# Performance work log

Hardware: AMD Instinct MI355X
Metric: run time of the kernel (lower is better)

The kernel has to match this reference:

```python
import jax, jax.numpy as jnp
import numpy as np

SEGMENT_LENGTHS = [1024, 2048, 4096]
DILATION_RATES = [1, 2, 4]


def setup_inputs() -> dict:
    key = jax.random.key(0)
    k1, k2, k3 = jax.random.split(key, 3)
    n = sum(SEGMENT_LENGTHS)  # 7168
    shape = (1, n, 8, 64)  # (b, n, h, d)
    q = jax.random.normal(k1, shape, dtype=jnp.float32)
    k = jax.random.normal(k2, shape, dtype=jnp.float32)
    v = jax.random.normal(k3, shape, dtype=jnp.float32)
    return {"q": q, "k": k, "v": v}


def _attend(q_seg, k_kv, v_kv):
    # q_seg: [b, q_len, h, d]; k_kv/v_kv: [b, k_len, h, d]
    d = q_seg.shape[-1]
    scale = 1.0 / jnp.sqrt(jnp.asarray(d, q_seg.dtype))
    scores = jnp.einsum("bqhd,bkhd->bhqk", q_seg, k_kv) * scale
    w = jax.nn.softmax(scores, axis=-1)
    return jnp.einsum("bhqk,bkhd->bqhd", w, v_kv)


def reference(q, k, v):
    # Single-device dilated attention (ring_size == 1, is_causal=False).
    n = q.shape[1]
    output = jnp.zeros_like(q)
    seg_start = 0
    for seg_len, dilation in zip(SEGMENT_LENGTHS, DILATION_RATES):
        if seg_start >= n:
            break
        seg_end = min(seg_start + seg_len, n)
        q_seg = q[:, seg_start:seg_end]
        if dilation > 1:
            k_d = k[:, ::dilation]
            v_d = v[:, ::dilation]
        else:
            k_d, v_d = k, v
        out_seg = _attend(q_seg, k_d, v_d)
        output = output.at[:, seg_start:seg_end].set(out_seg)
        seg_start = seg_end
    return output
```

## Files before the change

### kernel.cpp

```cpp
#include <hip/hip_runtime.h>

#define VB0 3670016L
#define VB1 7340032L
#define VB2 9175040L
#define WS_SHORTS 10092544L
#define PO_OFF 5046272L
#define PL_OFF (PO_OFF + 512L * 128 * 64)

typedef short bvec8 __attribute__((ext_vector_type(8)));
typedef float fvec16 __attribute__((ext_vector_type(16)));

static __device__ __forceinline__ short f2bf(float f) {
  unsigned u = __float_as_uint(f);
  u = u + 0x7fffu + ((u >> 16) & 1u);
  return (short)(u >> 16);
}
static __device__ __forceinline__ unsigned pk2(float a, float b) {
  unsigned ua = (__float_as_uint(a) + 0x8000u) >> 16;
  unsigned ub = (__float_as_uint(b) + 0x8000u) & 0xffff0000u;
  return ua | ub;
}
static __device__ __forceinline__ void async16(const short* g, short* l) {
  __builtin_amdgcn_global_load_lds((const __attribute__((address_space(1))) unsigned*)(void*)g,
                                   (__attribute__((address_space(3))) unsigned*)(void*)l, 16, 0, 0);
}

__global__ __launch_bounds__(256) void pack_all(const float* __restrict__ k,
                                                const float* __restrict__ v,
                                                short* __restrict__ W) {
  __shared__ float tl[64][65];
  int b = blockIdx.x, t = threadIdx.x;
  if (b < 896) {
    int h = b / 112, tile = b % 112, i0 = tile * 64;
    int r = t >> 2, c = t & 3;
    const float* src = k + ((long)(i0 + r) * 8 + h) * 64 + c * 16;
    short* dst = W + ((long)h * 7168 + i0 + r) * 64 + c * 16;
    short tmp[16] __attribute__((aligned(16)));
#pragma unroll
    for (int q4 = 0; q4 < 4; q4++) {
      float4 x = *(const float4*)(src + q4 * 4);
      tmp[q4 * 4 + 0] = f2bf(x.x); tmp[q4 * 4 + 1] = f2bf(x.y);
      tmp[q4 * 4 + 2] = f2bf(x.z); tmp[q4 * 4 + 3] = f2bf(x.w);
    }
    *(bvec8*)dst = *(const bvec8*)tmp;
    *(bvec8*)(dst + 8) = *(const bvec8*)(tmp + 8);
  } else {
    int b2 = b - 896;
    int h, tile, dil, L; long base;
    if (b2 < 896)       { L = 7168; dil = 1; h = b2 / 112; tile = b2 % 112; base = VB0; }
    else if (b2 < 1344) { int bb = b2 - 896;  L = 3584; dil = 2; h = bb / 56; tile = bb % 56; base = VB1; }
    else                { int bb = b2 - 1344; L = 1792; dil = 4; h = bb / 28; tile = bb % 28; base = VB2; }
    int i0 = tile * 64;
    int row = t >> 2, c = t & 3;
    const float* src = v + ((long)(i0 + row) * dil * 8 + h) * 64;
#pragma unroll
    for (int cc = 0; cc < 4; cc++) {
      int d0 = c * 16 + cc * 4;
      float4 x = *(const float4*)(src + d0);
      tl[row][d0 + 0] = x.x; tl[row][d0 + 1] = x.y;
      tl[row][d0 + 2] = x.z; tl[row][d0 + 3] = x.w;
    }
    __syncthreads();
    int d = t >> 2, part = t & 3;
    short tmp[16] __attribute__((aligned(16)));
#pragma unroll
    for (int u = 0; u < 16; u++) tmp[u] = f2bf(tl[part * 16 + u][d]);
    short* dst = W + base + ((long)h * 64 + d) * L + i0 + part * 16;
    *(bvec8*)dst = *(const bvec8*)tmp;
    *(bvec8*)(dst + 8) = *(const bvec8*)(tmp + 8);
  }
}

__global__ __launch_bounds__(256, 3) void attn_kern(const float* __restrict__ q,
                                                    const short* __restrict__ W,
                                                    float* __restrict__ out,
                                                    float* __restrict__ PO,
                                                    float* __restrict__ PL) {
  int b = blockIdx.x;
  int h, q0, dil, kt0, L; long vbo;
  if (b < 256)      { int sp = b & 3; h = (b >> 2) & 7; int qt = b >> 5;
                      q0 = qt * 128;        dil = 1; L = 7168; vbo = VB0; kt0 = sp * 28; }
  else if (b < 512) { int i = b - 256; int sp = i & 1; h = (i >> 1) & 7; int qt = i >> 4;
                      q0 = 1024 + qt * 128; dil = 2; L = 3584; vbo = VB1; kt0 = sp * 28; }
  else              { int i = b - 512; h = i & 7; int qt = i >> 3;
                      q0 = 3072 + qt * 128; dil = 4; L = 1792; vbo = VB2; kt0 = 0; }
  const short* kb = W + (long)h * 7168 * 64;
  const short* vt = W + vbo + (long)h * 64 * L;
  const int dil64 = dil * 64;

  __shared__ __attribute__((aligned(16))) short sK[2][4096];
  __shared__ __attribute__((aligned(16))) short sV[2][4096];
  short* sKf = &sK[0][0];
  short* sVf = &sV[0][0];

  int t = threadIdx.x, lane = t & 63, w = t >> 6;
  int ln = lane & 31, hb = lane >> 5;

  bvec8 qb[4];
  {
    const float* qp = q + ((long)(q0 + w * 32 + ln) * 8 + h) * 64 + 8 * hb;
    const float qs = 0.125f * 1.44269504088896f;
#pragma unroll
    for (int ks = 0; ks < 4; ks++)
#pragma unroll
      for (int j = 0; j < 8; j++)
        qb[ks][j] = f2bf(qs * qp[ks * 16 + j]);
  }

  int srow = lane >> 3, sch = (lane & 7) ^ srow;
  auto stage = [&](int keybase, int buf) {
#pragma unroll
    for (int r2 = 0; r2 < 2; r2++) {
      int row = (w * 2 + r2) * 8 + srow;
      const short* gpk = kb + (long)(keybase + row) * dil64 + sch * 8;
      async16(gpk, sKf + (long)buf * 4096 + (w * 2 + r2) * 512);
      const short* gpv = vt + (long)row * L + keybase + sch * 8;
      async16(gpv, sVf + (long)buf * 4096 + (w * 2 + r2) * 512);
    }
  };

  stage(kt0 * 64, 0);

  int koff[8];
#pragma unroll
  for (int ks = 0; ks < 4; ks++)
#pragma unroll
    for (int mb = 0; mb < 2; mb++)
      koff[ks * 2 + mb] = (mb * 32 + ln) * 64 + (((2 * ks + hb) ^ (ln & 7)) * 8);

  fvec16 Oa[2];
#pragma unroll
  for (int i = 0; i < 16; i++) { Oa[0][i] = 0.f; Oa[1][i] = 0.f; }
  float lp = 0.f;

  for (int it = 0; it < 28; it++) {
    int buf = it & 1;
    int key0 = (kt0 + it) * 64;
    __syncthreads();

    if (it < 27) stage(key0 + 64, buf ^ 1);

    fvec16 Sa[2];
#pragma unroll
    for (int i = 0; i < 16; i++) { Sa[0][i] = 0.f; Sa[1][i] = 0.f; }
    const short* sb = sKf + (long)buf * 4096;
#pragma unroll
    for (int ks = 0; ks < 4; ks++)
#pragma unroll
      for (int mb = 0; mb < 2; mb++) {
        bvec8 kf = *(const bvec8*)(sb + koff[ks * 2 + mb]);
        Sa[mb] = __builtin_amdgcn_mfma_f32_32x32x16_bf16(kf, qb[ks], Sa[mb], 0, 0, 0);
      }

    const short* vbuf = sVf + (long)buf * 4096;
    bvec8 vf[8];
#pragma unroll
    for (int ks = 0; ks < 4; ks++)
#pragma unroll
      for (int mb = 0; mb < 2; mb++)
        vf[mb * 4 + ks] = *(const bvec8*)(vbuf + koff[ks * 2 + mb]);

#pragma unroll
    for (int ks2 = 0; ks2 < 4; ks2++) {
      int mb = ks2 >> 1, r0i = (ks2 & 1) * 8;
      float p[8];
#pragma unroll
      for (int u = 0; u < 8; u++) {
        p[u] = __builtin_amdgcn_exp2f(Sa[mb][r0i + u]);
        lp += p[u];
      }
      unsigned da0 = pk2(p[0], p[1]), da1 = pk2(p[2], p[3]);
      unsigned db0 = pk2(p[4], p[5]), db1 = pk2(p[6], p[7]);
      unsigned s0 = hb ? da0 : db0, s1 = hb ? da1 : db1;
      unsigned x0 = __shfl_xor(s0, 32), x1 = __shfl_xor(s1, 32);
      union { unsigned u[4]; bvec8 v; } fu;
      fu.u[0] = hb ? x0 : da0;  fu.u[1] = hb ? x1 : da1;
      fu.u[2] = hb ? db0 : x0;  fu.u[3] = hb ? db1 : x1;
#pragma unroll
      for (int mb2 = 0; mb2 < 2; mb2++)
        Oa[mb2] = __builtin_amdgcn_mfma_f32_32x32x16_bf16(vf[mb2 * 4 + ks2], fu.v, Oa[mb2], 0, 0, 0);
    }
  }

  float lf = lp + __shfl_xor(lp, 32);
  int wl = w * 32 + ln;
  if (b < 512) {
    float* po = PO + ((long)b * 128 + wl) * 64;
#pragma unroll
    for (int mb2 = 0; mb2 < 2; mb2++)
#pragma unroll
      for (int r2 = 0; r2 < 4; r2++) {
        float4 x = { Oa[mb2][r2 * 4 + 0], Oa[mb2][r2 * 4 + 1],
                     Oa[mb2][r2 * 4 + 2], Oa[mb2][r2 * 4 + 3] };
        *(float4*)(po + mb2 * 32 + r2 * 8 + hb * 4) = x;
      }
    if (hb == 0) PL[(long)b * 128 + wl] = lf;
  } else {
    float inv = 1.f / lf;
    float* op = out + ((long)(q0 + wl) * 8 + h) * 64;
#pragma unroll
    for (int mb2 = 0; mb2 < 2; mb2++)
#pragma unroll
      for (int r2 = 0; r2 < 4; r2++) {
        float4 x = { Oa[mb2][r2 * 4 + 0] * inv, Oa[mb2][r2 * 4 + 1] * inv,
                     Oa[mb2][r2 * 4 + 2] * inv, Oa[mb2][r2 * 4 + 3] * inv };
        *(float4*)(op + mb2 * 32 + r2 * 8 + hb * 4) = x;
      }
  }
}

__global__ __launch_bounds__(256) void combine_kern(const float* __restrict__ PO,
                                                    const float* __restrict__ PL,
                                                    float* __restrict__ out) {
  int g = blockIdx.x, t = threadIdx.x;
  int base_b, nsp, q0, h;
  if (g < 64) { int qt = g >> 3; h = g & 7; base_b = qt * 32 + h * 4; nsp = 4; q0 = qt * 128; }
  else { int gi = g - 64; int qt = gi >> 3; h = gi & 7; base_b = 256 + qt * 16 + h * 2; nsp = 2; q0 = 1024 + qt * 128; }
  int r = t >> 1, ch = (t & 1) * 32;
  float lt = 0.f;
  for (int sp = 0; sp < nsp; sp++) lt += PL[(long)(base_b + sp) * 128 + r];
  float inv = 1.f / lt;
  float4 acc[8];
#pragma unroll
  for (int j = 0; j < 8; j++) { acc[j].x = 0.f; acc[j].y = 0.f; acc[j].z = 0.f; acc[j].w = 0.f; }
  for (int sp = 0; sp < nsp; sp++) {
    const float4* pb = (const float4*)(PO + ((long)(base_b + sp) * 128 + r) * 64 + ch);
#pragma unroll
    for (int j = 0; j < 8; j++) {
      float4 x = pb[j];
      acc[j].x += x.x; acc[j].y += x.y; acc[j].z += x.z; acc[j].w += x.w;
    }
  }
  float4* op = (float4*)(out + ((long)(q0 + r) * 8 + h) * 64 + ch);
#pragma unroll
  for (int j = 0; j < 8; j++) {
    float4 x = { acc[j].x * inv, acc[j].y * inv, acc[j].z * inv, acc[j].w * inv };
    op[j] = x;
  }
}

extern "C" void kernel_launch(void* const* d_in, const int* in_sizes, int n_in,
                              void* d_out, int out_size, void* d_ws, size_t ws_size,
                              hipStream_t stream) {
  const float* q = (const float*)d_in[0];
  const float* k = (const float*)d_in[1];
  const float* v = (const float*)d_in[2];
  float* out = (float*)d_out;
  short* W = (short*)d_ws;
  float* PO = (float*)d_ws + PO_OFF;
  float* PL = (float*)d_ws + PL_OFF;

  pack_all<<<2464, 256, 0, stream>>>(k, v, W);
  attn_kern<<<768, 256, 0, stream>>>(q, W, out, PO, PL);
  combine_kern<<<192, 256, 0, stream>>>(PO, PL, out);
}
```

Measured before the change: 160.9 us.

## Halve attention block to two waves, single-buffer V, split row-sum accumulators

The attention kernel now runs 128-thread blocks, each covering 64 query rows, so the grid doubles to 1536 blocks and the partial-output buffers and combine kernel are resized to match. V is single-buffered in shared memory: its fragments are loaded into registers before an added barrier, and only then is the next tile prefetched, which lowers LDS per block so more blocks fit per CU. The softmax row sum is split into four independent accumulators to shorten the dependency chain. The cost is an extra barrier per iteration, a less hidden V prefetch, and Q staging and partial writes repeated across twice as many blocks.

```diff
diff --git a/kernel.cpp b/kernel.cpp
--- a/kernel.cpp
+++ b/kernel.cpp
@@ -3,9 +3,8 @@
 #define VB0 3670016L
 #define VB1 7340032L
 #define VB2 9175040L
-#define WS_SHORTS 10092544L
 #define PO_OFF 5046272L
-#define PL_OFF (PO_OFF + 512L * 128 * 64)
+#define PL_OFF (PO_OFF + 1024L * 64 * 64)
 
 typedef short bvec8 __attribute__((ext_vector_type(8)));
 typedef float fvec16 __attribute__((ext_vector_type(16)));
@@ -71,27 +70,26 @@
   }
 }
 
-__global__ __launch_bounds__(256, 3) void attn_kern(const float* __restrict__ q,
+__global__ __launch_bounds__(128, 3) void attn_kern(const float* __restrict__ q,
                                                     const short* __restrict__ W,
                                                     float* __restrict__ out,
                                                     float* __restrict__ PO,
                                                     float* __restrict__ PL) {
   int b = blockIdx.x;
   int h, q0, dil, kt0, L; long vbo;
-  if (b < 256)      { int sp = b & 3; h = (b >> 2) & 7; int qt = b >> 5;
-                      q0 = qt * 128;        dil = 1; L = 7168; vbo = VB0; kt0 = sp * 28; }
-  else if (b < 512) { int i = b - 256; int sp = i & 1; h = (i >> 1) & 7; int qt = i >> 4;
-                      q0 = 1024 + qt * 128; dil = 2; L = 3584; vbo = VB1; kt0 = sp * 28; }
-  else              { int i = b - 512; h = i & 7; int qt = i >> 3;
-                      q0 = 3072 + qt * 128; dil = 4; L = 1792; vbo = VB2; kt0 = 0; }
+  if (b < 512)       { int sp = b & 3; h = (b >> 2) & 7; int qt = b >> 5;
+                       q0 = qt * 64;         dil = 1; L = 7168; vbo = VB0; kt0 = sp * 28; }
+  else if (b < 1024) { int i = b - 512; int sp = i & 1; h = (i >> 1) & 7; int qt = i >> 4;
+                       q0 = 1024 + qt * 64;  dil = 2; L = 3584; vbo = VB1; kt0 = sp * 28; }
+  else               { int i = b - 1024; h = i & 7; int qt = i >> 3;
+                       q0 = 3072 + qt * 64;  dil = 4; L = 1792; vbo = VB2; kt0 = 0; }
   const short* kb = W + (long)h * 7168 * 64;
   const short* vt = W + vbo + (long)h * 64 * L;
   const int dil64 = dil * 64;
 
   __shared__ __attribute__((aligned(16))) short sK[2][4096];
-  __shared__ __attribute__((aligned(16))) short sV[2][4096];
+  __shared__ __attribute__((aligned(16))) short sV[4096];
   short* sKf = &sK[0][0];
-  short* sVf = &sV[0][0];
 
   int t = threadIdx.x, lane = t & 63, w = t >> 6;
   int ln = lane & 31, hb = lane >> 5;
@@ -108,18 +106,25 @@
   }
 
   int srow = lane >> 3, sch = (lane & 7) ^ srow;
-  auto stage = [&](int keybase, int buf) {
-#pragma unroll
-    for (int r2 = 0; r2 < 2; r2++) {
-      int row = (w * 2 + r2) * 8 + srow;
+  auto stageK = [&](int keybase, int buf) {
+#pragma unroll
+    for (int r2 = 0; r2 < 4; r2++) {
+      int g = w * 4 + r2, row = g * 8 + srow;
       const short* gpk = kb + (long)(keybase + row) * dil64 + sch * 8;
-      async16(gpk, sKf + (long)buf * 4096 + (w * 2 + r2) * 512);
+      async16(gpk, sKf + (long)buf * 4096 + g * 512);
+    }
+  };
+  auto stageV = [&](int keybase) {
+#pragma unroll
+    for (int r2 = 0; r2 < 4; r2++) {
+      int g = w * 4 + r2, row = g * 8 + srow;
       const short* gpv = vt + (long)row * L + keybase + sch * 8;
-      async16(gpv, sVf + (long)buf * 4096 + (w * 2 + r2) * 512);
+      async16(gpv, &sV[g * 512]);
     }
   };
 
-  stage(kt0 * 64, 0);
+  stageK(kt0 * 64, 0);
+  stageV(kt0 * 64);
 
   int koff[8];
 #pragma unroll
@@ -131,14 +136,23 @@
   fvec16 Oa[2];
 #pragma unroll
   for (int i = 0; i < 16; i++) { Oa[0][i] = 0.f; Oa[1][i] = 0.f; }
-  float lp = 0.f;
+  float lp4[4] = {0.f, 0.f, 0.f, 0.f};
 
   for (int it = 0; it < 28; it++) {
     int buf = it & 1;
     int key0 = (kt0 + it) * 64;
     __syncthreads();
 
-    if (it < 27) stage(key0 + 64, buf ^ 1);
+    bvec8 vf[8];
+#pragma unroll
+    for (int ks = 0; ks < 4; ks++)
+#pragma unroll
+      for (int mb = 0; mb < 2; mb++)
+        vf[mb * 4 + ks] = *(const bvec8*)(&sV[0] + koff[ks * 2 + mb]);
+
+    __syncthreads();
+
+    if (it < 27) { stageK(key0 + 64, buf ^ 1); stageV(key0 + 64); }
 
     fvec16 Sa[2];
 #pragma unroll
@@ -152,14 +166,6 @@
         Sa[mb] = __builtin_amdgcn_mfma_f32_32x32x16_bf16(kf, qb[ks], Sa[mb], 0, 0, 0);
       }
 
-    const short* vbuf = sVf + (long)buf * 4096;
-    bvec8 vf[8];
-#pragma unroll
-    for (int ks = 0; ks < 4; ks++)
-#pragma unroll
-      for (int mb = 0; mb < 2; mb++)
-        vf[mb * 4 + ks] = *(const bvec8*)(vbuf + koff[ks * 2 + mb]);
-
 #pragma unroll
     for (int ks2 = 0; ks2 < 4; ks2++) {
       int mb = ks2 >> 1, r0i = (ks2 & 1) * 8;
@@ -167,7 +173,7 @@
 #pragma unroll
       for (int u = 0; u < 8; u++) {
         p[u] = __builtin_amdgcn_exp2f(Sa[mb][r0i + u]);
-        lp += p[u];
+        lp4[ks2] += p[u];
       }
       unsigned da0 = pk2(p[0], p[1]), da1 = pk2(p[2], p[3]);
       unsigned db0 = pk2(p[4], p[5]), db1 = pk2(p[6], p[7]);
@@ -182,10 +188,11 @@
     }
   }
 
+  float lp = (lp4[0] + lp4[1]) + (lp4[2] + lp4[3]);
   float lf = lp + __shfl_xor(lp, 32);
   int wl = w * 32 + ln;
-  if (b < 512) {
-    float* po = PO + ((long)b * 128 + wl) * 64;
+  if (b < 1024) {
+    float* po = PO + ((long)b * 64 + wl) * 64;
 #pragma unroll
     for (int mb2 = 0; mb2 < 2; mb2++)
 #pragma unroll
@@ -194,7 +201,7 @@
                      Oa[mb2][r2 * 4 + 2], Oa[mb2][r2 * 4 + 3] };
         *(float4*)(po + mb2 * 32 + r2 * 8 + hb * 4) = x;
       }
-    if (hb == 0) PL[(long)b * 128 + wl] = lf;
+    if (hb == 0) PL[(long)b * 64 + wl] = lf;
   } else {
     float inv = 1.f / lf;
     float* op = out + ((long)(q0 + wl) * 8 + h) * 64;
@@ -214,26 +221,26 @@
                                                     float* __restrict__ out) {
   int g = blockIdx.x, t = threadIdx.x;
   int base_b, nsp, q0, h;
-  if (g < 64) { int qt = g >> 3; h = g & 7; base_b = qt * 32 + h * 4; nsp = 4; q0 = qt * 128; }
-  else { int gi = g - 64; int qt = gi >> 3; h = gi & 7; base_b = 256 + qt * 16 + h * 2; nsp = 2; q0 = 1024 + qt * 128; }
-  int r = t >> 1, ch = (t & 1) * 32;
+  if (g < 128) { int qt = g >> 3; h = g & 7; base_b = qt * 32 + h * 4;        nsp = 4; q0 = qt * 64; }
+  else { int gi = g - 128; int qt = gi >> 3; h = gi & 7; base_b = 512 + qt * 16 + h * 2; nsp = 2; q0 = 1024 + qt * 64; }
+  int r = t >> 2, d0 = (t & 3) * 16;
   float lt = 0.f;
-  for (int sp = 0; sp < nsp; sp++) lt += PL[(long)(base_b + sp) * 128 + r];
+  for (int sp = 0; sp < nsp; sp++) lt += PL[(long)(base_b + sp) * 64 + r];
   float inv = 1.f / lt;
-  float4 acc[8];
-#pragma unroll
-  for (int j = 0; j < 8; j++) { acc[j].x = 0.f; acc[j].y = 0.f; acc[j].z = 0.f; acc[j].w = 0.f; }
+  float4 acc[4];
+#pragma unroll
+  for (int j = 0; j < 4; j++) { acc[j].x = 0.f; acc[j].y = 0.f; acc[j].z = 0.f; acc[j].w = 0.f; }
   for (int sp = 0; sp < nsp; sp++) {
-    const float4* pb = (const float4*)(PO + ((long)(base_b + sp) * 128 + r) * 64 + ch);
-#pragma unroll
-    for (int j = 0; j < 8; j++) {
+    const float4* pb = (const float4*)(PO + ((long)(base_b + sp) * 64 + r) * 64 + d0);
+#pragma unroll
+    for (int j = 0; j < 4; j++) {
       float4 x = pb[j];
       acc[j].x += x.x; acc[j].y += x.y; acc[j].z += x.z; acc[j].w += x.w;
     }
   }
-  float4* op = (float4*)(out + ((long)(q0 + r) * 8 + h) * 64 + ch);
-#pragma unroll
-  for (int j = 0; j < 8; j++) {
+  float4* op = (float4*)(out + ((long)(q0 + r) * 8 + h) * 64 + d0);
+#pragma unroll
+  for (int j = 0; j < 4; j++) {
     float4 x = { acc[j].x * inv, acc[j].y * inv, acc[j].z * inv, acc[j].w * inv };
     op[j] = x;
   }
@@ -251,6 +258,6 @@
   float* PL = (float*)d_ws + PL_OFF;
 
   pack_all<<<2464, 256, 0, stream>>>(k, v, W);
-  attn_kern<<<768, 256, 0, stream>>>(q, W, out, PO, PL);
-  combine_kern<<<192, 256, 0, stream>>>(PO, PL, out);
-}
+  attn_kern<<<1536, 128, 0, stream>>>(q, W, out, PO, PL);
+  combine_kern<<<384, 256, 0, stream>>>(PO, PL, out);
+}
```

Measured after the change: 164.0 us. About the same (+1.9%).
